# Kernel tuning notes

Hardware: AMD Instinct MI355X
Metric: run time of the kernel (lower is better)

Reference implementation:

```python
import jax, jax.numpy as jnp
import numpy as np

D_MODEL = 4096
N_HEADS = 32
KV_HEADS = 8
HEAD_DIM = D_MODEL // N_HEADS  # 128
GROUPS = N_HEADS // KV_HEADS   # 4
ROPE_THETA = 500000.0
CLIP_QKV = 8.0
SEQLENS = [512, 768, 384, 384]
T = sum(SEQLENS)  # 2048 total ragged tokens


def setup_inputs() -> dict:
    key = jax.random.key(0)
    k1, k2, k3 = jax.random.split(key, 3)
    hidden_states = jax.random.normal(k1, (T, D_MODEL), dtype=jnp.float32)
    # fused Wqkv: rows = d_model (Q) + 2 * kv_heads * head_dim (K,V)
    w_qkv = jax.random.normal(k2, (D_MODEL + 2 * KV_HEADS * HEAD_DIM, D_MODEL), dtype=jnp.float32) * 0.02
    w_o = jax.random.normal(k3, (D_MODEL, D_MODEL), dtype=jnp.float32) * 0.02
    # ragged-batch metadata: cumulative sequence lengths, per-token positions
    cu = np.concatenate([[0], np.cumsum(SEQLENS)]).astype(np.int32)
    pos = np.concatenate([np.arange(l) for l in SEQLENS]).astype(np.float32)
    inv_freq = 1.0 / (ROPE_THETA ** (np.arange(0, HEAD_DIM, 2, dtype=np.float32) / HEAD_DIM))  # [64]
    freqs = pos[:, None] * inv_freq[None, :]  # [T, 64]
    return {
        "hidden_states": hidden_states,
        "w_qkv": w_qkv,
        "w_o": w_o,
        "cos": jnp.asarray(np.cos(freqs), dtype=jnp.float32),
        "sin": jnp.asarray(np.sin(freqs), dtype=jnp.float32),
        "cu_seqlens": jnp.asarray(cu),
    }


def _rope(x, cos, sin):
    # rotate-half (NeoX-style) RoPE, as in TGI PositionRotaryEmbedding
    h = HEAD_DIM // 2
    x1, x2 = x[..., :h], x[..., h:]
    c = cos[:, None, :]  # [T,1,h] broadcast over heads
    s = sin[:, None, :]
    return jnp.concatenate([x1 * c - x2 * s, x2 * c + x1 * s], axis=-1)


def reference(hidden_states, w_qkv, w_o, cos, sin, cu_seqlens):
    # fused QKV projection + clip_qkv clamp
    qkv = jnp.clip(hidden_states @ w_qkv.T, -CLIP_QKV, CLIP_QKV)  # [T, 6144]
    q_sz = N_HEADS * HEAD_DIM
    kv_sz = KV_HEADS * HEAD_DIM
    q = qkv[:, :q_sz].reshape(T, N_HEADS, HEAD_DIM)
    k = qkv[:, q_sz:q_sz + kv_sz].reshape(T, KV_HEADS, HEAD_DIM)
    v = qkv[:, q_sz + kv_sz:].reshape(T, KV_HEADS, HEAD_DIM)
    q = _rope(q, cos, sin)
    k = _rope(k, cos, sin)
    # GQA: expand kv heads to query heads (kv_head_mapping = repeat_interleave)
    kr = jnp.repeat(k, GROUPS, axis=1)  # [T, H, D]
    vr = jnp.repeat(v, GROUPS, axis=1)
    # varlen causal mask: same segment AND key index <= query index
    idx = jnp.arange(T)
    seg = jnp.searchsorted(cu_seqlens, idx, side="right") - 1  # [T]
    mask = (seg[:, None] == seg[None, :]) & (idx[:, None] >= idx[None, :])  # [T,T]
    scale = HEAD_DIM ** -0.5
    scores = jnp.einsum("qhd,khd->hqk", q, kr) * scale  # [H,T,T]
    scores = jnp.where(mask[None, :, :], scores, jnp.finfo(scores.dtype).min)
    attn = jax.nn.softmax(scores, axis=-1)
    out = jnp.einsum("hqk,khd->qhd", attn, vr).reshape(T, N_HEADS * HEAD_DIM)
    return out @ w_o.T
```

## Files before the change

kernel.cpp:

```cpp
#include <hip/hip_runtime.h>

#define T_TOK 2048
#define DM    4096
#define NH    32
#define KVH   8
#define HD    128
#define QKV_N 6144
#define KOFF  4096
#define VOFF  5120
#define SCALE 0.08838834764831845f

typedef __attribute__((ext_vector_type(8))) short  short8;
typedef __attribute__((ext_vector_type(4))) float  floatx4;

__device__ __forceinline__ ushort f2bf(float f) {
  union { float f; unsigned u; } x; x.f = f;
  unsigned u = x.u;
  return (ushort)((u + 0x7fffu + ((u >> 16) & 1u)) >> 16);
}
__device__ __forceinline__ float bf2f(ushort h) {
  union { unsigned u; float f; } x; x.u = ((unsigned)h) << 16;
  return x.f;
}

__global__ void __launch_bounds__(256) cast_bf16_kernel(const float* __restrict__ x,
                                                        ushort* __restrict__ y, int n4) {
  int i = blockIdx.x * 256 + threadIdx.x;
  if (i >= n4) return;
  float4 v = ((const float4*)x)[i];
  ushort4 o;
  o.x = f2bf(v.x); o.y = f2bf(v.y); o.z = f2bf(v.z); o.w = f2bf(v.w);
  ((ushort4*)y)[i] = o;
}

__device__ __forceinline__ void gld_lds16(const ushort* g, ushort* l) {
  __builtin_amdgcn_global_load_lds((const __attribute__((address_space(1))) unsigned int*)g,
                                   (__attribute__((address_space(3))) unsigned int*)l,
                                   16, 0, 0);
}

template <int MLO, int NLO>
__device__ __forceinline__ void mfma_quad(floatx4 (&acc)[8][4],
                                          const short8 (&afr)[4][2],
                                          const short8 (&bfr)[4][2]) {
  __builtin_amdgcn_s_setprio(1);
#pragma unroll
  for (int ks = 0; ks < 2; ++ks)
#pragma unroll
    for (int mi = 0; mi < 4; ++mi)
#pragma unroll
      for (int ni = 0; ni < 2; ++ni)
        acc[MLO + mi][NLO + ni] = __builtin_amdgcn_mfma_f32_16x16x32_bf16(
            afr[mi][ks], bfr[NLO + ni][ks], acc[MLO + mi][NLO + ni], 0, 0, 0);
  __builtin_amdgcn_s_setprio(0);
}

__device__ __forceinline__ void stage_half(const ushort* __restrict__ G, size_t row0,
                                           int K, int k0, ushort* lbase, int tid) {
#pragma unroll
  for (int j = 0; j < 2; ++j) {
    int row   = j * 64 + (tid >> 3);
    int chunk = (tid & 7) ^ (row & 7);
    gld_lds16(G + (row0 + (size_t)row) * K + k0 + chunk * 8,
              lbase + (size_t)(j * 512 + tid) * 8);
  }
}

__global__ void __launch_bounds__(512, 2)
gemm256(const ushort* __restrict__ A, const ushort* __restrict__ B,
        ushort* __restrict__ Cb, float* __restrict__ Cf, int N, int K, int mode) {
  __shared__ __align__(16) ushort As[2][2][128][64];
  __shared__ __align__(16) ushort Bs[2][2][128][64];

  const int tid = threadIdx.x;
  const int lane = tid & 63, wv = tid >> 6;
  const int r = lane & 15, g = lane >> 4;
  const int wm = wv >> 2, wn = wv & 3;

  const int nwg = (int)gridDim.x;
  const int wg  = (int)blockIdx.x;
  const int wgs = (wg & 7) * (nwg >> 3) + (wg >> 3);
  const int nbx = N >> 8;
  const int bx = wgs % nbx, by = wgs / nbx;
  const int bm = by * 256, bn = bx * 256;

  const int NT = K >> 6;

  floatx4 acc[8][4];
#pragma unroll
  for (int mi = 0; mi < 8; ++mi)
#pragma unroll
    for (int ni = 0; ni < 4; ++ni) acc[mi][ni] = (floatx4){0.f, 0.f, 0.f, 0.f};

  stage_half(B, bn,       K, 0, &Bs[0][0][0][0], tid);
  stage_half(B, bn + 128, K, 0, &Bs[0][1][0][0], tid);
  stage_half(A, bm,       K, 0, &As[0][0][0][0], tid);
  stage_half(A, bm + 128, K, 0, &As[0][1][0][0], tid);
  if (NT > 1) {
    stage_half(B, bn,       K, 64, &Bs[1][0][0][0], tid);
    stage_half(B, bn + 128, K, 64, &Bs[1][1][0][0], tid);
    stage_half(A, bm,       K, 64, &As[1][0][0][0], tid);
    asm volatile("s_waitcnt vmcnt(6)");
  } else {
    asm volatile("s_waitcnt vmcnt(0)");
  }
  __builtin_amdgcn_s_barrier();

  short8 afr[4][2], bfr[4][2];
  const int cswz = (r & 7) << 3;

  for (int t = 0; t < NT; ++t) {
    const int buf = t & 1;
    const ushort* Ab = &As[buf][wm][0][0];
    const ushort* Bb = &Bs[buf][wn >> 1][0][0];
    const int brow = (wn & 1) * 64;

#pragma unroll
    for (int ni = 0; ni < 2; ++ni)
#pragma unroll
      for (int ks = 0; ks < 2; ++ks)
        bfr[ni][ks] = *(const short8*)&Bb[(brow + ni * 16 + r) * 64 +
                                          ((ks * 32 + g * 8) ^ cswz)];
#pragma unroll
    for (int m = 0; m < 4; ++m)
#pragma unroll
      for (int ks = 0; ks < 2; ++ks)
        afr[m][ks] = *(const short8*)&Ab[(m * 16 + r) * 64 +
                                         ((ks * 32 + g * 8) ^ cswz)];
    if (t + 1 < NT) stage_half(A, bm + 128, K, (t + 1) * 64, &As[(t + 1) & 1][1][0][0], tid);
    __builtin_amdgcn_s_barrier();
    mfma_quad<0, 0>(acc, afr, bfr);
    __builtin_amdgcn_s_barrier();

#pragma unroll
    for (int ni = 2; ni < 4; ++ni)
#pragma unroll
      for (int ks = 0; ks < 2; ++ks)
        bfr[ni][ks] = *(const short8*)&Bb[(brow + ni * 16 + r) * 64 +
                                          ((ks * 32 + g * 8) ^ cswz)];
    __builtin_amdgcn_s_barrier();
    mfma_quad<0, 2>(acc, afr, bfr);
    __builtin_amdgcn_s_barrier();

#pragma unroll
    for (int m = 0; m < 4; ++m)
#pragma unroll
      for (int ks = 0; ks < 2; ++ks)
        afr[m][ks] = *(const short8*)&Ab[((64 + m * 16) + r) * 64 +
                                         ((ks * 32 + g * 8) ^ cswz)];
    if (t + 2 < NT) stage_half(B, bn, K, (t + 2) * 64, &Bs[buf][0][0][0], tid);
    __builtin_amdgcn_s_barrier();
    mfma_quad<4, 2>(acc, afr, bfr);
    __builtin_amdgcn_s_barrier();

    if (t + 2 < NT) {
      stage_half(B, bn + 128, K, (t + 2) * 64, &Bs[buf][1][0][0], tid);
      stage_half(A, bm,       K, (t + 2) * 64, &As[buf][0][0][0], tid);
    }
    if (t < NT - 2) asm volatile("s_waitcnt vmcnt(6)");
    else            asm volatile("s_waitcnt vmcnt(0)");
    __builtin_amdgcn_s_barrier();
    mfma_quad<4, 0>(acc, afr, bfr);
    __builtin_amdgcn_s_barrier();
  }

#pragma unroll
  for (int mi = 0; mi < 8; ++mi)
#pragma unroll
    for (int v = 0; v < 4; ++v) {
      int row = bm + wm * 128 + mi * 16 + g * 4 + v;
#pragma unroll
      for (int ni = 0; ni < 4; ++ni) {
        int col = bn + wn * 64 + ni * 16 + r;
        float x = acc[mi][ni][v];
        if (mode == 0) {
          x = fminf(8.0f, fmaxf(-8.0f, x));
          Cb[(size_t)row * N + col] = f2bf(x);
        } else {
          Cf[(size_t)row * N + col] = x;
        }
      }
    }
}

__global__ void __launch_bounds__(256) rope_kernel(ushort* __restrict__ qkv,
                                                   const float* __restrict__ cosb,
                                                   const float* __restrict__ sinb) {
  int t = blockIdx.y;
  int h = blockIdx.x * 4 + (threadIdx.x >> 6);
  int d = threadIdx.x & 63;
  size_t base = (size_t)t * QKV_N + (h < NH ? h * HD : KOFF + (h - NH) * HD);
  float x1 = bf2f(qkv[base + d]);
  float x2 = bf2f(qkv[base + 64 + d]);
  float c = cosb[t * 64 + d], s = sinb[t * 64 + d];
  float y1 = x1 * c - x2 * s;
  float y2 = x2 * c + x1 * s;
  if (h < NH) { y1 *= SCALE; y2 *= SCALE; }
  qkv[base + d]      = f2bf(y1);
  qkv[base + 64 + d] = f2bf(y2);
}

__global__ void __launch_bounds__(256) vtrans_kernel(const ushort* __restrict__ qkv,
                                                     ushort* __restrict__ vt) {
  int idx = blockIdx.x * 256 + threadIdx.x;
  int t  = idx & (T_TOK - 1);
  int d  = (idx >> 11) & (HD - 1);
  int kv = idx >> 18;
  vt[idx] = qkv[(size_t)t * QKV_N + VOFF + kv * HD + d];
}

__global__ void __launch_bounds__(256) attn_kernel(const ushort* __restrict__ qkv,
                                                   const ushort* __restrict__ vt,
                                                   ushort* __restrict__ o) {
  __shared__ ushort Ks[64][136];
  __shared__ ushort Vts[128][72];
  __shared__ ushort Ps[4][16][72];

  const int tid = threadIdx.x, wave = tid >> 6, lane = tid & 63;
  const int r = lane & 15, g = lane >> 4;
  const int qtile = blockIdx.x, head = blockIdx.y, kvh = head >> 2;
  const int q0 = qtile * 64;
  int s0;
  if (q0 < 512) s0 = 0; else if (q0 < 1280) s0 = 512;
  else if (q0 < 1664) s0 = 1280; else s0 = 1664;

  short8 qf[4];
  const int qrow = q0 + wave * 16 + r;
#pragma unroll
  for (int ks = 0; ks < 4; ks++)
    qf[ks] = *(const short8*)&qkv[(size_t)qrow * QKV_N + head * HD + ks * 32 + g * 8];

  floatx4 zero = {0.f, 0.f, 0.f, 0.f};
  floatx4 oacc[8];
#pragma unroll
  for (int b = 0; b < 8; b++) oacc[b] = zero;
  float mrun[4] = {-1e30f, -1e30f, -1e30f, -1e30f};
  float lrun[4] = {0.f, 0.f, 0.f, 0.f};

  const size_t kcol  = (size_t)KOFF + kvh * HD;
  const size_t vbase = (size_t)kvh * HD * T_TOK;

  for (int k0 = s0; k0 < q0 + 64; k0 += 64) {
    short8 kreg[4], vreg[4];
#pragma unroll
    for (int p = 0; p < 4; p++) {
      int krow = p * 16 + (tid >> 4), kc = (tid & 15) * 8;
      kreg[p] = *(const short8*)&qkv[(size_t)(k0 + krow) * QKV_N + kcol + kc];
      int vd = p * 32 + (tid >> 3), vc = (tid & 7) * 8;
      vreg[p] = *(const short8*)&vt[vbase + (size_t)vd * T_TOK + k0 + vc];
    }
    __syncthreads();
#pragma unroll
    for (int p = 0; p < 4; p++) {
      int krow = p * 16 + (tid >> 4), kc = (tid & 15) * 8;
      *(short8*)&Ks[krow][kc] = kreg[p];
      int vd = p * 32 + (tid >> 3), vc = (tid & 7) * 8;
      *(short8*)&Vts[vd][vc] = vreg[p];
    }
    __syncthreads();

    floatx4 sacc[4];
#pragma unroll
    for (int s = 0; s < 4; s++) sacc[s] = zero;
#pragma unroll
    for (int s = 0; s < 4; s++)
#pragma unroll
      for (int ks = 0; ks < 4; ks++) {
        short8 kf = *(const short8*)&Ks[s * 16 + r][ks * 32 + g * 8];
        sacc[s] = __builtin_amdgcn_mfma_f32_16x16x32_bf16(qf[ks], kf, sacc[s], 0, 0, 0);
      }

    const bool diag = (k0 == q0);
    float sv[4][4];
#pragma unroll
    for (int s = 0; s < 4; s++)
#pragma unroll
      for (int v = 0; v < 4; v++) {
        float x = sacc[s][v];
        if (diag) {
          int ka = k0 + s * 16 + r;
          int qa = q0 + wave * 16 + g * 4 + v;
          if (ka > qa) x = -1e30f;
        }
        sv[s][v] = x;
      }

    float rmax[4];
#pragma unroll
    for (int v = 0; v < 4; v++)
      rmax[v] = fmaxf(fmaxf(sv[0][v], sv[1][v]), fmaxf(sv[2][v], sv[3][v]));
#pragma unroll
    for (int off = 1; off < 16; off <<= 1)
#pragma unroll
      for (int v = 0; v < 4; v++)
        rmax[v] = fmaxf(rmax[v], __shfl_xor(rmax[v], off, 64));

    float newm[4], alpha[4];
#pragma unroll
    for (int v = 0; v < 4; v++) {
      newm[v]  = fmaxf(mrun[v], rmax[v]);
      alpha[v] = __expf(mrun[v] - newm[v]);
      mrun[v]  = newm[v];
    }

    float pv[4][4];
    float rsum[4] = {0.f, 0.f, 0.f, 0.f};
#pragma unroll
    for (int s = 0; s < 4; s++)
#pragma unroll
      for (int v = 0; v < 4; v++) {
        float p = __expf(sv[s][v] - newm[v]);
        pv[s][v] = p;
        rsum[v] += p;
      }
#pragma unroll
    for (int off = 1; off < 16; off <<= 1)
#pragma unroll
      for (int v = 0; v < 4; v++)
        rsum[v] += __shfl_xor(rsum[v], off, 64);
#pragma unroll
    for (int v = 0; v < 4; v++) lrun[v] = lrun[v] * alpha[v] + rsum[v];
#pragma unroll
    for (int b = 0; b < 8; b++)
#pragma unroll
      for (int v = 0; v < 4; v++) oacc[b][v] *= alpha[v];

#pragma unroll
    for (int s = 0; s < 4; s++)
#pragma unroll
      for (int v = 0; v < 4; v++)
        Ps[wave][g * 4 + v][s * 16 + r] = f2bf(pv[s][v]);
    __syncthreads();

    short8 pf0 = *(const short8*)&Ps[wave][r][g * 8];
    short8 pf1 = *(const short8*)&Ps[wave][r][32 + g * 8];

#pragma unroll
    for (int b = 0; b < 8; b++) {
      short8 v0 = *(const short8*)&Vts[b * 16 + r][g * 8];
      short8 v1 = *(const short8*)&Vts[b * 16 + r][32 + g * 8];
      oacc[b] = __builtin_amdgcn_mfma_f32_16x16x32_bf16(pf0, v0, oacc[b], 0, 0, 0);
      oacc[b] = __builtin_amdgcn_mfma_f32_16x16x32_bf16(pf1, v1, oacc[b], 0, 0, 0);
    }
  }

  float rinv[4];
#pragma unroll
  for (int v = 0; v < 4; v++) rinv[v] = 1.0f / lrun[v];
#pragma unroll
  for (int b = 0; b < 8; b++)
#pragma unroll
    for (int v = 0; v < 4; v++) {
      int qa = q0 + wave * 16 + g * 4 + v;
      o[(size_t)qa * DM + head * HD + b * 16 + r] = f2bf(oacc[b][v] * rinv[v]);
    }
}

extern "C" void kernel_launch(void* const* d_in, const int* in_sizes, int n_in,
                              void* d_out, int out_size, void* d_ws, size_t ws_size,
                              hipStream_t stream) {
  const float* hs   = (const float*)d_in[0];
  const float* wqkv = (const float*)d_in[1];
  const float* wo   = (const float*)d_in[2];
  const float* cosb = (const float*)d_in[3];
  const float* sinb = (const float*)d_in[4];
  float* out = (float*)d_out;

  char* w = (char*)d_ws;
  ushort* h_bf   = (ushort*)(w);
  ushort* wq_bf  = (ushort*)(w + 16777216);
  ushort* wo_bf  = (ushort*)(w + 67108864);
  ushort* qkv_bf = (ushort*)(w + 100663296);
  ushort* vt     = (ushort*)(w + 125829120);
  ushort* ao_bf  = (ushort*)(w + 130023424);

  cast_bf16_kernel<<<8192,  256, 0, stream>>>(hs,   h_bf,  2097152);
  cast_bf16_kernel<<<24576, 256, 0, stream>>>(wqkv, wq_bf, 6291456);
  cast_bf16_kernel<<<16384, 256, 0, stream>>>(wo,   wo_bf, 4194304);

  gemm256<<<dim3(192), 512, 0, stream>>>(h_bf, wq_bf, qkv_bf, nullptr, QKV_N, DM, 0);
  rope_kernel<<<dim3(10, T_TOK), 256, 0, stream>>>(qkv_bf, cosb, sinb);
  vtrans_kernel<<<8192, 256, 0, stream>>>(qkv_bf, vt);
  attn_kernel<<<dim3(32, 32), 256, 0, stream>>>(qkv_bf, vt, ao_bf);
  gemm256<<<dim3(128), 512, 0, stream>>>(ao_bf, wo_bf, nullptr, out, DM, DM, 1);
}
```

Measured before the change: 567.6 us.

## Split-K the output projection GEMM into two halves and reduce with an add kernel

The output projection GEMM launched only 128 workgroups on a GPU with 256 CUs, leaving half the machine idle. It now splits K into two halves, giving 256 workgroups that each write a float32 partial to workspace, and a separate elementwise kernel sums the two partials into the output. The main loop is also unrolled by two through a macro so buffer selection is compile-time. The cost is 64MB of extra partial-sum traffic plus one more launch, and the partial buffer reuses workspace that held the already-consumed bf16 inputs.

Measured after the change: 550.6 us. 3.0% less time.

```diff
diff --git a/kernel.cpp b/kernel.cpp
--- a/kernel.cpp
+++ b/kernel.cpp
@@ -33,6 +33,15 @@
   ((ushort4*)y)[i] = o;
 }
 
+__global__ void __launch_bounds__(256) add_f32_kernel(const float4* __restrict__ a,
+                                                      const float4* __restrict__ b,
+                                                      float4* __restrict__ o, int n4) {
+  int i = blockIdx.x * 256 + threadIdx.x;
+  if (i >= n4) return;
+  float4 x = a[i], y = b[i];
+  o[i] = make_float4(x.x + y.x, x.y + y.y, x.z + y.z, x.w + y.w);
+}
+
 __device__ __forceinline__ void gld_lds16(const ushort* g, ushort* l) {
   __builtin_amdgcn_global_load_lds((const __attribute__((address_space(1))) unsigned int*)g,
                                    (__attribute__((address_space(3))) unsigned int*)l,
@@ -66,9 +75,59 @@
   }
 }
 
+#define TILE(BUF, tt)                                                             \
+  do {                                                                            \
+    const ushort* Ab = (BUF) ? Ab1 : Ab0;                                         \
+    const ushort* Bb = (BUF) ? Bb1 : Bb0;                                         \
+        \
+    _Pragma("unroll") for (int ni = 0; ni < 2; ++ni)                              \
+      _Pragma("unroll") for (int ks = 0; ks < 2; ++ks)                            \
+        bfr[ni][ks] = *(const short8*)&Bb[(brow + ni * 16 + r) * 64 +             \
+                                          ((ks * 32 + g * 8) ^ cswz)];            \
+    _Pragma("unroll") for (int m = 0; m < 4; ++m)                                 \
+      _Pragma("unroll") for (int ks = 0; ks < 2; ++ks)                            \
+        afr[m][ks] = *(const short8*)&Ab[(m * 16 + r) * 64 +                      \
+                                         ((ks * 32 + g * 8) ^ cswz)];             \
+    if ((tt) + 1 < NT)                                                            \
+      stage_half(A, bm + 128, K, koff + ((tt) + 1) * 64,                          \
+                 &As[1 - (BUF)][1][0][0], tid);                                   \
+    __builtin_amdgcn_s_barrier();                                                 \
+    mfma_quad<0, 0>(acc, afr, bfr);                                               \
+    __builtin_amdgcn_s_barrier();                                                 \
+        \
+    _Pragma("unroll") for (int ni = 2; ni < 4; ++ni)                              \
+      _Pragma("unroll") for (int ks = 0; ks < 2; ++ks)                            \
+        bfr[ni][ks] = *(const short8*)&Bb[(brow + ni * 16 + r) * 64 +             \
+                                          ((ks * 32 + g * 8) ^ cswz)];            \
+    __builtin_amdgcn_s_barrier();                                                 \
+    mfma_quad<0, 2>(acc, afr, bfr);                                               \
+    __builtin_amdgcn_s_barrier();                                                 \
+        \
+    _Pragma("unroll") for (int m = 0; m < 4; ++m)                                 \
+      _Pragma("unroll") for (int ks = 0; ks < 2; ++ks)                            \
+        afr[m][ks] = *(const short8*)&Ab[((64 + m * 16) + r) * 64 +               \
+                                         ((ks * 32 + g * 8) ^ cswz)];             \
+    if ((tt) + 2 < NT)                                                            \
+      stage_half(B, bn, K, koff + ((tt) + 2) * 64, &Bs[BUF][0][0][0], tid);       \
+    __builtin_amdgcn_s_barrier();                                                 \
+    mfma_quad<4, 2>(acc, afr, bfr);                                               \
+    __builtin_amdgcn_s_barrier();                                                 \
+        \
+    if ((tt) + 2 < NT) {                                                          \
+      stage_half(B, bn + 128, K, koff + ((tt) + 2) * 64, &Bs[BUF][1][0][0], tid); \
+      stage_half(A, bm, K, koff + ((tt) + 2) * 64, &As[BUF][0][0][0], tid);       \
+    }                                                                             \
+    if ((tt) < NT - 2) asm volatile("s_waitcnt vmcnt(6)");                        \
+    else               asm volatile("s_waitcnt vmcnt(0)");                        \
+    __builtin_amdgcn_s_barrier();                                                 \
+    mfma_quad<4, 0>(acc, afr, bfr);                                               \
+    __builtin_amdgcn_s_barrier();                                                 \
+  } while (0)
+
 __global__ void __launch_bounds__(512, 2)
 gemm256(const ushort* __restrict__ A, const ushort* __restrict__ B,
-        ushort* __restrict__ Cb, float* __restrict__ Cf, int N, int K, int mode) {
+        ushort* __restrict__ Cb, float* __restrict__ Cf,
+        int N, int K, int Kloc, int KS, int mode) {
   __shared__ __align__(16) ushort As[2][2][128][64];
   __shared__ __align__(16) ushort Bs[2][2][128][64];
 
@@ -81,10 +140,14 @@
   const int wg  = (int)blockIdx.x;
   const int wgs = (wg & 7) * (nwg >> 3) + (wg >> 3);
   const int nbx = N >> 8;
-  const int bx = wgs % nbx, by = wgs / nbx;
+  const int by  = wgs / (nbx * KS);
+  const int rem = wgs - by * nbx * KS;
+  const int bx  = rem / KS;
+  const int ks_ = rem - bx * KS;
   const int bm = by * 256, bn = bx * 256;
-
-  const int NT = K >> 6;
+  const int koff = ks_ * Kloc;
+
+  const int NT = Kloc >> 6;
 
   floatx4 acc[8][4];
 #pragma unroll
@@ -92,14 +155,14 @@
 #pragma unroll
     for (int ni = 0; ni < 4; ++ni) acc[mi][ni] = (floatx4){0.f, 0.f, 0.f, 0.f};
 
-  stage_half(B, bn,       K, 0, &Bs[0][0][0][0], tid);
-  stage_half(B, bn + 128, K, 0, &Bs[0][1][0][0], tid);
-  stage_half(A, bm,       K, 0, &As[0][0][0][0], tid);
-  stage_half(A, bm + 128, K, 0, &As[0][1][0][0], tid);
+  stage_half(B, bn,       K, koff, &Bs[0][0][0][0], tid);
+  stage_half(B, bn + 128, K, koff, &Bs[0][1][0][0], tid);
+  stage_half(A, bm,       K, koff, &As[0][0][0][0], tid);
+  stage_half(A, bm + 128, K, koff, &As[0][1][0][0], tid);
   if (NT > 1) {
-    stage_half(B, bn,       K, 64, &Bs[1][0][0][0], tid);
-    stage_half(B, bn + 128, K, 64, &Bs[1][1][0][0], tid);
-    stage_half(A, bm,       K, 64, &As[1][0][0][0], tid);
+    stage_half(B, bn,       K, koff + 64, &Bs[1][0][0][0], tid);
+    stage_half(B, bn + 128, K, koff + 64, &Bs[1][1][0][0], tid);
+    stage_half(A, bm,       K, koff + 64, &As[1][0][0][0], tid);
     asm volatile("s_waitcnt vmcnt(6)");
   } else {
     asm volatile("s_waitcnt vmcnt(0)");
@@ -108,62 +171,18 @@
 
   short8 afr[4][2], bfr[4][2];
   const int cswz = (r & 7) << 3;
-
-  for (int t = 0; t < NT; ++t) {
-    const int buf = t & 1;
-    const ushort* Ab = &As[buf][wm][0][0];
-    const ushort* Bb = &Bs[buf][wn >> 1][0][0];
-    const int brow = (wn & 1) * 64;
-
-#pragma unroll
-    for (int ni = 0; ni < 2; ++ni)
-#pragma unroll
-      for (int ks = 0; ks < 2; ++ks)
-        bfr[ni][ks] = *(const short8*)&Bb[(brow + ni * 16 + r) * 64 +
-                                          ((ks * 32 + g * 8) ^ cswz)];
-#pragma unroll
-    for (int m = 0; m < 4; ++m)
-#pragma unroll
-      for (int ks = 0; ks < 2; ++ks)
-        afr[m][ks] = *(const short8*)&Ab[(m * 16 + r) * 64 +
-                                         ((ks * 32 + g * 8) ^ cswz)];
-    if (t + 1 < NT) stage_half(A, bm + 128, K, (t + 1) * 64, &As[(t + 1) & 1][1][0][0], tid);
-    __builtin_amdgcn_s_barrier();
-    mfma_quad<0, 0>(acc, afr, bfr);
-    __builtin_amdgcn_s_barrier();
-
-#pragma unroll
-    for (int ni = 2; ni < 4; ++ni)
-#pragma unroll
-      for (int ks = 0; ks < 2; ++ks)
-        bfr[ni][ks] = *(const short8*)&Bb[(brow + ni * 16 + r) * 64 +
-                                          ((ks * 32 + g * 8) ^ cswz)];
-    __builtin_amdgcn_s_barrier();
-    mfma_quad<0, 2>(acc, afr, bfr);
-    __builtin_amdgcn_s_barrier();
-
-#pragma unroll
-    for (int m = 0; m < 4; ++m)
-#pragma unroll
-      for (int ks = 0; ks < 2; ++ks)
-        afr[m][ks] = *(const short8*)&Ab[((64 + m * 16) + r) * 64 +
-                                         ((ks * 32 + g * 8) ^ cswz)];
-    if (t + 2 < NT) stage_half(B, bn, K, (t + 2) * 64, &Bs[buf][0][0][0], tid);
-    __builtin_amdgcn_s_barrier();
-    mfma_quad<4, 2>(acc, afr, bfr);
-    __builtin_amdgcn_s_barrier();
-
-    if (t + 2 < NT) {
-      stage_half(B, bn + 128, K, (t + 2) * 64, &Bs[buf][1][0][0], tid);
-      stage_half(A, bm,       K, (t + 2) * 64, &As[buf][0][0][0], tid);
-    }
-    if (t < NT - 2) asm volatile("s_waitcnt vmcnt(6)");
-    else            asm volatile("s_waitcnt vmcnt(0)");
-    __builtin_amdgcn_s_barrier();
-    mfma_quad<4, 0>(acc, afr, bfr);
-    __builtin_amdgcn_s_barrier();
+  const int brow = (wn & 1) * 64;
+  const ushort* Ab0 = &As[0][wm][0][0];
+  const ushort* Ab1 = &As[1][wm][0][0];
+  const ushort* Bb0 = &Bs[0][wn >> 1][0][0];
+  const ushort* Bb1 = &Bs[1][wn >> 1][0][0];
+
+  for (int t = 0; t < NT; t += 2) {
+    TILE(0, t);
+    TILE(1, t + 1);
   }
 
+  float* Cfo = Cf + (size_t)ks_ * ((size_t)2048 * N);
 #pragma unroll
   for (int mi = 0; mi < 8; ++mi)
 #pragma unroll
@@ -177,7 +196,7 @@
           x = fminf(8.0f, fmaxf(-8.0f, x));
           Cb[(size_t)row * N + col] = f2bf(x);
         } else {
-          Cf[(size_t)row * N + col] = x;
+          Cfo[(size_t)row * N + col] = x;
         }
       }
     }
@@ -373,14 +392,20 @@
   ushort* qkv_bf = (ushort*)(w + 100663296);
   ushort* vt     = (ushort*)(w + 125829120);
   ushort* ao_bf  = (ushort*)(w + 130023424);
+  float*  part   = (float*)(w);
 
   cast_bf16_kernel<<<8192,  256, 0, stream>>>(hs,   h_bf,  2097152);
   cast_bf16_kernel<<<24576, 256, 0, stream>>>(wqkv, wq_bf, 6291456);
   cast_bf16_kernel<<<16384, 256, 0, stream>>>(wo,   wo_bf, 4194304);
 
-  gemm256<<<dim3(192), 512, 0, stream>>>(h_bf, wq_bf, qkv_bf, nullptr, QKV_N, DM, 0);
+  gemm256<<<dim3(192), 512, 0, stream>>>(h_bf, wq_bf, qkv_bf, nullptr,
+                                         QKV_N, DM, DM, 1, 0);
   rope_kernel<<<dim3(10, T_TOK), 256, 0, stream>>>(qkv_bf, cosb, sinb);
   vtrans_kernel<<<8192, 256, 0, stream>>>(qkv_bf, vt);
   attn_kernel<<<dim3(32, 32), 256, 0, stream>>>(qkv_bf, vt, ao_bf);
-  gemm256<<<dim3(128), 512, 0, stream>>>(ao_bf, wo_bf, nullptr, out, DM, DM, 1);
-}
+  gemm256<<<dim3(256), 512, 0, stream>>>(ao_bf, wo_bf, nullptr, part,
+                                         DM, DM, 2048, 2, 1);
+  add_f32_kernel<<<8192, 256, 0, stream>>>((const float4*)part,
+                                           (const float4*)(part + (size_t)2048 * 4096),
+                                           (float4*)out, 2097152);
+}
```

## Split-K the output projection and load attention K/V fragments directly from global

Applied to the files above, without the earlier changes.

The output-projection GEMM is split along K into two halves, launching 256 workgroups instead of 128 to fill more CUs. The halves write fp32 partials into workspace, and a separate add kernel sums them. The attention kernel drops its LDS staging of K and V, and each wave now reads MFMA fragments straight from global/L2, with raised wave priority around the MFMAs. This removes two block-wide syncs per tile, but costs extra global traffic: a 64MB partial write and read for the split-K, and redundant per-wave K/V loads.

Measured after the change: 664.7 us. +17.1%, slower.

```diff
diff --git a/kernel.cpp b/kernel.cpp
--- a/kernel.cpp
+++ b/kernel.cpp
@@ -33,6 +33,15 @@
   ((ushort4*)y)[i] = o;
 }
 
+__global__ void __launch_bounds__(256) add_f32_kernel(const float4* __restrict__ a,
+                                                      const float4* __restrict__ b,
+                                                      float4* __restrict__ o, int n4) {
+  int i = blockIdx.x * 256 + threadIdx.x;
+  if (i >= n4) return;
+  float4 x = a[i], y = b[i];
+  o[i] = make_float4(x.x + y.x, x.y + y.y, x.z + y.z, x.w + y.w);
+}
+
 __device__ __forceinline__ void gld_lds16(const ushort* g, ushort* l) {
   __builtin_amdgcn_global_load_lds((const __attribute__((address_space(1))) unsigned int*)g,
                                    (__attribute__((address_space(3))) unsigned int*)l,
@@ -68,7 +77,8 @@
 
 __global__ void __launch_bounds__(512, 2)
 gemm256(const ushort* __restrict__ A, const ushort* __restrict__ B,
-        ushort* __restrict__ Cb, float* __restrict__ Cf, int N, int K, int mode) {
+        ushort* __restrict__ Cb, float* __restrict__ Cf,
+        int N, int K, int Kloc, int KS, int mode) {
   __shared__ __align__(16) ushort As[2][2][128][64];
   __shared__ __align__(16) ushort Bs[2][2][128][64];
 
@@ -81,10 +91,14 @@
   const int wg  = (int)blockIdx.x;
   const int wgs = (wg & 7) * (nwg >> 3) + (wg >> 3);
   const int nbx = N >> 8;
-  const int bx = wgs % nbx, by = wgs / nbx;
+  const int by  = wgs / (nbx * KS);
+  const int rem = wgs - by * nbx * KS;
+  const int bx  = rem / KS;
+  const int ks_ = rem - bx * KS;
   const int bm = by * 256, bn = bx * 256;
-
-  const int NT = K >> 6;
+  const int koff = ks_ * Kloc;
+
+  const int NT = Kloc >> 6;
 
   floatx4 acc[8][4];
 #pragma unroll
@@ -92,14 +106,14 @@
 #pragma unroll
     for (int ni = 0; ni < 4; ++ni) acc[mi][ni] = (floatx4){0.f, 0.f, 0.f, 0.f};
 
-  stage_half(B, bn,       K, 0, &Bs[0][0][0][0], tid);
-  stage_half(B, bn + 128, K, 0, &Bs[0][1][0][0], tid);
-  stage_half(A, bm,       K, 0, &As[0][0][0][0], tid);
-  stage_half(A, bm + 128, K, 0, &As[0][1][0][0], tid);
+  stage_half(B, bn,       K, koff, &Bs[0][0][0][0], tid);
+  stage_half(B, bn + 128, K, koff, &Bs[0][1][0][0], tid);
+  stage_half(A, bm,       K, koff, &As[0][0][0][0], tid);
+  stage_half(A, bm + 128, K, koff, &As[0][1][0][0], tid);
   if (NT > 1) {
-    stage_half(B, bn,       K, 64, &Bs[1][0][0][0], tid);
-    stage_half(B, bn + 128, K, 64, &Bs[1][1][0][0], tid);
-    stage_half(A, bm,       K, 64, &As[1][0][0][0], tid);
+    stage_half(B, bn,       K, koff + 64, &Bs[1][0][0][0], tid);
+    stage_half(B, bn + 128, K, koff + 64, &Bs[1][1][0][0], tid);
+    stage_half(A, bm,       K, koff + 64, &As[1][0][0][0], tid);
     asm volatile("s_waitcnt vmcnt(6)");
   } else {
     asm volatile("s_waitcnt vmcnt(0)");
@@ -107,7 +121,7 @@
   __builtin_amdgcn_s_barrier();
 
   short8 afr[4][2], bfr[4][2];
-  const int cswz = (r & 7) << 3;
+  const int cswz = (r & 15 & 7) << 3;
 
   for (int t = 0; t < NT; ++t) {
     const int buf = t & 1;
@@ -127,7 +141,8 @@
       for (int ks = 0; ks < 2; ++ks)
         afr[m][ks] = *(const short8*)&Ab[(m * 16 + r) * 64 +
                                          ((ks * 32 + g * 8) ^ cswz)];
-    if (t + 1 < NT) stage_half(A, bm + 128, K, (t + 1) * 64, &As[(t + 1) & 1][1][0][0], tid);
+    if (t + 1 < NT) stage_half(A, bm + 128, K, koff + (t + 1) * 64,
+                               &As[(t + 1) & 1][1][0][0], tid);
     __builtin_amdgcn_s_barrier();
     mfma_quad<0, 0>(acc, afr, bfr);
     __builtin_amdgcn_s_barrier();
@@ -148,14 +163,14 @@
       for (int ks = 0; ks < 2; ++ks)
         afr[m][ks] = *(const short8*)&Ab[((64 + m * 16) + r) * 64 +
                                          ((ks * 32 + g * 8) ^ cswz)];
-    if (t + 2 < NT) stage_half(B, bn, K, (t + 2) * 64, &Bs[buf][0][0][0], tid);
+    if (t + 2 < NT) stage_half(B, bn, K, koff + (t + 2) * 64, &Bs[buf][0][0][0], tid);
     __builtin_amdgcn_s_barrier();
     mfma_quad<4, 2>(acc, afr, bfr);
     __builtin_amdgcn_s_barrier();
 
     if (t + 2 < NT) {
-      stage_half(B, bn + 128, K, (t + 2) * 64, &Bs[buf][1][0][0], tid);
-      stage_half(A, bm,       K, (t + 2) * 64, &As[buf][0][0][0], tid);
+      stage_half(B, bn + 128, K, koff + (t + 2) * 64, &Bs[buf][1][0][0], tid);
+      stage_half(A, bm,       K, koff + (t + 2) * 64, &As[buf][0][0][0], tid);
     }
     if (t < NT - 2) asm volatile("s_waitcnt vmcnt(6)");
     else            asm volatile("s_waitcnt vmcnt(0)");
@@ -164,6 +179,7 @@
     __builtin_amdgcn_s_barrier();
   }
 
+  float* Cfo = Cf + (size_t)ks_ * ((size_t)2048 * N);
 #pragma unroll
   for (int mi = 0; mi < 8; ++mi)
 #pragma unroll
@@ -177,7 +193,7 @@
           x = fminf(8.0f, fmaxf(-8.0f, x));
           Cb[(size_t)row * N + col] = f2bf(x);
         } else {
-          Cf[(size_t)row * N + col] = x;
+          Cfo[(size_t)row * N + col] = x;
         }
       }
     }
@@ -212,8 +228,6 @@
 __global__ void __launch_bounds__(256) attn_kernel(const ushort* __restrict__ qkv,
                                                    const ushort* __restrict__ vt,
                                                    ushort* __restrict__ o) {
-  __shared__ ushort Ks[64][136];
-  __shared__ ushort Vts[128][72];
   __shared__ ushort Ps[4][16][72];
 
   const int tid = threadIdx.x, wave = tid >> 6, lane = tid & 63;
@@ -241,34 +255,22 @@
   const size_t vbase = (size_t)kvh * HD * T_TOK;
 
   for (int k0 = s0; k0 < q0 + 64; k0 += 64) {
-    short8 kreg[4], vreg[4];
-#pragma unroll
-    for (int p = 0; p < 4; p++) {
-      int krow = p * 16 + (tid >> 4), kc = (tid & 15) * 8;
-      kreg[p] = *(const short8*)&qkv[(size_t)(k0 + krow) * QKV_N + kcol + kc];
-      int vd = p * 32 + (tid >> 3), vc = (tid & 7) * 8;
-      vreg[p] = *(const short8*)&vt[vbase + (size_t)vd * T_TOK + k0 + vc];
-    }
-    __syncthreads();
-#pragma unroll
-    for (int p = 0; p < 4; p++) {
-      int krow = p * 16 + (tid >> 4), kc = (tid & 15) * 8;
-      *(short8*)&Ks[krow][kc] = kreg[p];
-      int vd = p * 32 + (tid >> 3), vc = (tid & 7) * 8;
-      *(short8*)&Vts[vd][vc] = vreg[p];
-    }
-    __syncthreads();
-
     floatx4 sacc[4];
 #pragma unroll
     for (int s = 0; s < 4; s++) sacc[s] = zero;
 #pragma unroll
-    for (int s = 0; s < 4; s++)
-#pragma unroll
-      for (int ks = 0; ks < 4; ks++) {
-        short8 kf = *(const short8*)&Ks[s * 16 + r][ks * 32 + g * 8];
-        sacc[s] = __builtin_amdgcn_mfma_f32_16x16x32_bf16(qf[ks], kf, sacc[s], 0, 0, 0);
-      }
+    for (int s = 0; s < 4; s++) {
+      short8 kf[4];
+#pragma unroll
+      for (int ks = 0; ks < 4; ks++)
+        kf[ks] = *(const short8*)&qkv[(size_t)(k0 + s * 16 + r) * QKV_N +
+                                      kcol + ks * 32 + g * 8];
+      __builtin_amdgcn_s_setprio(1);
+#pragma unroll
+      for (int ks = 0; ks < 4; ks++)
+        sacc[s] = __builtin_amdgcn_mfma_f32_16x16x32_bf16(qf[ks], kf[ks], sacc[s], 0, 0, 0);
+      __builtin_amdgcn_s_setprio(0);
+    }
 
     const bool diag = (k0 == q0);
     float sv[4][4];
@@ -330,17 +332,18 @@
 #pragma unroll
       for (int v = 0; v < 4; v++)
         Ps[wave][g * 4 + v][s * 16 + r] = f2bf(pv[s][v]);
-    __syncthreads();
 
     short8 pf0 = *(const short8*)&Ps[wave][r][g * 8];
     short8 pf1 = *(const short8*)&Ps[wave][r][32 + g * 8];
 
 #pragma unroll
     for (int b = 0; b < 8; b++) {
-      short8 v0 = *(const short8*)&Vts[b * 16 + r][g * 8];
-      short8 v1 = *(const short8*)&Vts[b * 16 + r][32 + g * 8];
+      short8 v0 = *(const short8*)&vt[vbase + (size_t)(b * 16 + r) * T_TOK + k0 + g * 8];
+      short8 v1 = *(const short8*)&vt[vbase + (size_t)(b * 16 + r) * T_TOK + k0 + 32 + g * 8];
+      __builtin_amdgcn_s_setprio(1);
       oacc[b] = __builtin_amdgcn_mfma_f32_16x16x32_bf16(pf0, v0, oacc[b], 0, 0, 0);
       oacc[b] = __builtin_amdgcn_mfma_f32_16x16x32_bf16(pf1, v1, oacc[b], 0, 0, 0);
+      __builtin_amdgcn_s_setprio(0);
     }
   }
 
@@ -373,14 +376,20 @@
   ushort* qkv_bf = (ushort*)(w + 100663296);
   ushort* vt     = (ushort*)(w + 125829120);
   ushort* ao_bf  = (ushort*)(w + 130023424);
+  float*  part   = (float*)(w);
 
   cast_bf16_kernel<<<8192,  256, 0, stream>>>(hs,   h_bf,  2097152);
   cast_bf16_kernel<<<24576, 256, 0, stream>>>(wqkv, wq_bf, 6291456);
   cast_bf16_kernel<<<16384, 256, 0, stream>>>(wo,   wo_bf, 4194304);
 
-  gemm256<<<dim3(192), 512, 0, stream>>>(h_bf, wq_bf, qkv_bf, nullptr, QKV_N, DM, 0);
+  gemm256<<<dim3(192), 512, 0, stream>>>(h_bf, wq_bf, qkv_bf, nullptr,
+                                         QKV_N, DM, DM, 1, 0);
   rope_kernel<<<dim3(10, T_TOK), 256, 0, stream>>>(qkv_bf, cosb, sinb);
   vtrans_kernel<<<8192, 256, 0, stream>>>(qkv_bf, vt);
   attn_kernel<<<dim3(32, 32), 256, 0, stream>>>(qkv_bf, vt, ao_bf);
-  gemm256<<<dim3(128), 512, 0, stream>>>(ao_bf, wo_bf, nullptr, out, DM, DM, 1);
-}
+  gemm256<<<dim3(256), 512, 0, stream>>>(ao_bf, wo_bf, nullptr, part,
+                                         DM, DM, 2048, 2, 1);
+  add_f32_kernel<<<8192, 256, 0, stream>>>((const float4*)part,
+                                           (const float4*)(part + (size_t)2048 * 4096),
+                                           (float4*)out, 2097152);
+}
```
